# Kernel optimization log

Measured on AMD Instinct MI355X. Metric: run time of the kernel, lower is better.

The kernel has to match this reference:

```python
import jax, jax.numpy as jnp
import numpy as np

B, N, NIN = 32, 128, 64
MSG_HID, MSG_OUT, N_HID, N_OUT = 256, 64, 256, 64
E = N * (N - 1)  # fully connected, no self loops


def setup_inputs() -> dict:
    key = jax.random.key(0)
    ks = jax.random.split(key, 12)

    # one-hot incidence matrices (NRI convention)
    off = np.ones((N, N), dtype=np.float32) - np.eye(N, dtype=np.float32)
    recv_idx, send_idx = np.where(off)
    eye = np.eye(N, dtype=np.float32)
    rel_rec = jnp.asarray(eye[recv_idx])    # [E, N]
    rel_send = jnp.asarray(eye[send_idx])   # [E, N]

    s = 0.05
    inp = {
        "inputs": jax.random.normal(ks[0], (B, N, NIN), jnp.float32),
        "rel_rec": rel_rec,
        "rel_send": rel_send,
        "rel_types": jax.random.uniform(ks[1], (B, E, 2), jnp.float32),
        "msg_fc1_w": jax.random.normal(ks[2], (MSG_HID, 2 * NIN), jnp.float32) * s,
        "msg_fc1_b": jnp.zeros((MSG_HID,), jnp.float32),
        "msg_fc2_w": jax.random.normal(ks[3], (MSG_OUT, MSG_HID), jnp.float32) * s,
        "msg_fc2_b": jnp.zeros((MSG_OUT,), jnp.float32),
        "out_fc1_w": jax.random.normal(ks[4], (N_HID, MSG_OUT), jnp.float32) * s,
        "out_fc1_b": jnp.zeros((N_HID,), jnp.float32),
        "out_fc2_w": jax.random.normal(ks[5], (N_HID, N_HID), jnp.float32) * s,
        "out_fc2_b": jnp.zeros((N_HID,), jnp.float32),
        "out_fc3_w": jax.random.normal(ks[6], (N_OUT, N_HID), jnp.float32) * s,
        "out_fc3_b": jnp.zeros((N_OUT,), jnp.float32),
    }
    return inp


def reference(inputs, rel_rec, rel_send, rel_types,
              msg_fc1_w, msg_fc1_b, msg_fc2_w, msg_fc2_b,
              out_fc1_w, out_fc1_b, out_fc2_w, out_fc2_b,
              out_fc3_w, out_fc3_b):
    # node2edge: gather sender / receiver node features via one-hot matmul
    senders = jnp.einsum('en,bnf->bef', rel_send, inputs)    # [B,E,NIN]
    receivers = jnp.einsum('en,bnf->bef', rel_rec, inputs)   # [B,E,NIN]
    pre_msg = jnp.concatenate([senders, receivers], axis=-1)  # [B,E,2*NIN]

    all_msgs = jnp.zeros(pre_msg.shape[:2] + (MSG_OUT,), pre_msg.dtype)
    for i in range(2):  # edge-type loop (shared weights, as in the original)
        msg = jax.nn.relu(pre_msg @ msg_fc1_w.T + msg_fc1_b)
        msg = jax.nn.relu(msg @ msg_fc2_w.T + msg_fc2_b)
        all_msgs = all_msgs + msg * rel_types[:, :, i:i + 1]

    # edge2node: scatter-add messages to receiving nodes
    agg_msgs = jnp.einsum('bem,en->bnm', all_msgs, rel_rec)   # [B,N,MSG_OUT]

    pred = jax.nn.relu(agg_msgs @ out_fc1_w.T + out_fc1_b)
    pred = jax.nn.relu(pred @ out_fc2_w.T + out_fc2_b)
    pred = pred @ out_fc3_w.T + out_fc3_b                      # [B,N,N_OUT]
    return pred
```

## Files before the change

kernel.cpp:

```cpp
#include <hip/hip_runtime.h>

#define BB 32
#define NN_ 128
#define NIN 64
#define MH 256
#define MO 64
#define NH 256
#define NO 64
#define EDGES 16256

typedef __attribute__((ext_vector_type(8))) short short8;
typedef __attribute__((ext_vector_type(4))) float f32x4;
typedef __attribute__((ext_vector_type(2))) float f32x2;


static __device__ __forceinline__ unsigned short f2bf(float f) {
    unsigned u = __float_as_uint(f);
    u = (u + 0x7fffu + ((u >> 16) & 1u)) >> 16;
    return (unsigned short)u;
}

static __device__ __forceinline__ unsigned bf_pack(float lo, float hi) {
    return __builtin_amdgcn_perm(__float_as_uint(hi) + 0x8000u,
                                 __float_as_uint(lo) + 0x8000u, 0x07060302u);
}

static __device__ __forceinline__ short8 pack8(float4 f0, float4 f1) {
    uint4 u;
    u.x = bf_pack(f0.x, f0.y);
    u.y = bf_pack(f0.z, f0.w);
    u.z = bf_pack(f1.x, f1.y);
    u.w = bf_pack(f1.z, f1.w);
    return __builtin_bit_cast(short8, u);
}

static __device__ __forceinline__ void unpack8v(uint4 u, f32x2* f) {
    f[0] = (f32x2){__uint_as_float(u.x << 16), __uint_as_float(u.x & 0xffff0000u)};
    f[1] = (f32x2){__uint_as_float(u.y << 16), __uint_as_float(u.y & 0xffff0000u)};
    f[2] = (f32x2){__uint_as_float(u.z << 16), __uint_as_float(u.z & 0xffff0000u)};
    f[3] = (f32x2){__uint_as_float(u.w << 16), __uint_as_float(u.w & 0xffff0000u)};
}

static __device__ __forceinline__ short8 buildAv(const f32x2* s, const f32x2* p) {
    uint4 u;
    #pragma unroll
    for (int i = 0; i < 4; ++i) {
        f32x2 h = s[i] + p[i];
        h = __builtin_elementwise_max(h, (f32x2){0.f, 0.f});
        ((unsigned*)&u)[i] = bf_pack(h.x, h.y);
    }
    return __builtin_bit_cast(short8, u);
}

__global__ __launch_bounds__(256) void prep_kernel(
    const float* __restrict__ x, const float* __restrict__ W1,
    const float* __restrict__ b1, const float* __restrict__ W2,
    const float* __restrict__ O1, const float* __restrict__ O2,
    const float* __restrict__ O3,
    unsigned short* __restrict__ psb, unsigned short* __restrict__ prb,
    unsigned short* __restrict__ w2b, unsigned short* __restrict__ o1b,
    unsigned short* __restrict__ o2b, unsigned short* __restrict__ o3b)
{
    int blk = blockIdx.x;
    int t = threadIdx.x;
    if (blk < 256) {
        int row0 = blk << 4;
        int b = blk >> 3;
        int w = t >> 6, lane = t & 63, ml = lane & 15, q = lane >> 4;

        short8 aX[2];
        #pragma unroll
        for (int s = 0; s < 2; ++s) {
            const float* base = x + (size_t)(row0 + ml) * NIN + s * 32 + q * 8;
            aX[s] = pack8(*(const float4*)base, *(const float4*)(base + 4));
        }

        #pragma unroll
        for (int half = 0; half < 2; ++half) {
            #pragma unroll
            for (int nt = 0; nt < 4; ++nt) {
                int col = w * 64 + nt * 16 + ml;
                const float* wrow = W1 + (size_t)col * (2 * NIN) + half * 64 + q * 8;
                f32x4 acc = (f32x4){0.f, 0.f, 0.f, 0.f};
                #pragma unroll
                for (int s = 0; s < 2; ++s) {
                    short8 bw = pack8(*(const float4*)(wrow + 32 * s),
                                      *(const float4*)(wrow + 32 * s + 4));
                    acc = __builtin_amdgcn_mfma_f32_16x16x32_bf16(aX[s], bw, acc, 0, 0, 0);
                }
                if (half == 0) {
                    #pragma unroll
                    for (int reg = 0; reg < 4; ++reg) {
                        int n = (row0 + q * 4 + reg) & 127;
                        psb[((size_t)(b * 32 + (col >> 3)) * NN_ + n) * 8 + (col & 7)]
                            = f2bf(acc[reg]);
                    }
                } else {
                    float bv = b1[col];
                    #pragma unroll
                    for (int reg = 0; reg < 4; ++reg) {
                        int n = (row0 + q * 4 + reg) & 127;
                        prb[((size_t)(b * NN_) + n) * MH + col] = f2bf(acc[reg] + bv);
                    }
                }
            }
        }
    } else if (blk < 320) {
        int i = ((blk - 256) << 8) + t;
        int kc4 = i >> 9, rem = i & 511;
        int n = rem >> 3, k7 = i & 7;
        w2b[i] = f2bf(W2[n * MH + kc4 * 8 + k7]);
    } else {
        int i = ((blk - 320) << 8) + t;
        if (i < 16384)       o1b[i]         = f2bf(O1[i]);
        else if (i < 81920)  o2b[i - 16384] = f2bf(O2[i - 16384]);
        else                 o3b[i - 81920] = f2bf(O3[i - 81920]);
    }
}

__global__ __launch_bounds__(256, 4) void edge_kernel(
    const float* __restrict__ rt, const float* __restrict__ b2,
    const unsigned short* __restrict__ psb, const unsigned short* __restrict__ prb,
    const unsigned short* __restrict__ w2b, float* __restrict__ agg)
{
    int blk = blockIdx.x;
    int b = blk & 31;
    int r0 = (blk >> 5) << 1;
    int tid = threadIdx.x;
    int w = tid >> 6, lane = tid & 63, ml = lane & 15, q = lane >> 4;

    __shared__ float rtw_lds[2][128];
    __shared__ float red[2][4][64];
    {
        int rr = tid >> 7, s = tid & 127;
        int r = r0 + rr;
        float v = 0.f;
        if (s != r) {
            int e = r * 127 + s - (s > r ? 1 : 0);
            const float* p = rt + ((size_t)(b * EDGES + e)) * 2;
            v = __builtin_nontemporal_load(p) + __builtin_nontemporal_load(p + 1);
        }
        rtw_lds[rr][s] = v;
    }
    __syncthreads();

    int slot0 = 32 * w + ml;
    int slot1 = slot0 + 16;

    const uint4* ps4 = (const uint4*)psb + (size_t)b * (32 * NN_);
    const uint4* pr4_0 = (const uint4*)(prb + ((size_t)(b * NN_ + r0)) * MH);
    const uint4* pr4_1 = (const uint4*)(prb + ((size_t)(b * NN_ + r0 + 1)) * MH);
    const uint4* w24 = (const uint4*)w2b;

    f32x4 acc[2][2][4];
    #pragma unroll
    for (int rr = 0; rr < 2; ++rr)
        #pragma unroll
        for (int mt = 0; mt < 2; ++mt)
            #pragma unroll
            for (int nt = 0; nt < 4; ++nt)
                acc[rr][mt][nt] = (f32x4){0.f, 0.f, 0.f, 0.f};

    #pragma unroll
    for (int kc = 0; kc < 8; ++kc) {
        int kc4 = 4 * kc + q;
        uint4 us0 = ps4[kc4 * NN_ + slot0];
        uint4 us1 = ps4[kc4 * NN_ + slot1];
        uint4 up0 = pr4_0[kc4];
        uint4 up1 = pr4_1[kc4];

        f32x2 s0f[4], s1f[4], p0f[4], p1f[4];
        unpack8v(us0, s0f); unpack8v(us1, s1f);
        unpack8v(up0, p0f); unpack8v(up1, p1f);

        short8 a00 = buildAv(s0f, p0f);
        short8 a01 = buildAv(s1f, p0f);
        short8 a10 = buildAv(s0f, p1f);
        short8 a11 = buildAv(s1f, p1f);

        #pragma unroll
        for (int nt = 0; nt < 4; ++nt) {
            short8 bw = __builtin_bit_cast(short8, w24[kc4 * 64 + 16 * nt + ml]);
            acc[0][0][nt] = __builtin_amdgcn_mfma_f32_16x16x32_bf16(a00, bw, acc[0][0][nt], 0, 0, 0);
            acc[0][1][nt] = __builtin_amdgcn_mfma_f32_16x16x32_bf16(a01, bw, acc[0][1][nt], 0, 0, 0);
            acc[1][0][nt] = __builtin_amdgcn_mfma_f32_16x16x32_bf16(a10, bw, acc[1][0][nt], 0, 0, 0);
            acc[1][1][nt] = __builtin_amdgcn_mfma_f32_16x16x32_bf16(a11, bw, acc[1][1][nt], 0, 0, 0);
        }
    }

    float b2c[4];
    #pragma unroll
    for (int nt = 0; nt < 4; ++nt) b2c[nt] = b2[16 * nt + ml];

    #pragma unroll
    for (int rr = 0; rr < 2; ++rr) {
        float colsum[4] = {0.f, 0.f, 0.f, 0.f};
        #pragma unroll
        for (int mt = 0; mt < 2; ++mt) {
            int slotbase = 32 * w + 16 * mt + 4 * q;
            #pragma unroll
            for (int reg = 0; reg < 4; ++reg) {
                float rw = rtw_lds[rr][slotbase + reg];
                #pragma unroll
                for (int nt = 0; nt < 4; ++nt)
                    colsum[nt] += fmaxf(acc[rr][mt][nt][reg] + b2c[nt], 0.f) * rw;
            }
        }
        #pragma unroll
        for (int nt = 0; nt < 4; ++nt) {
            colsum[nt] += __shfl_xor(colsum[nt], 16);
            colsum[nt] += __shfl_xor(colsum[nt], 32);
        }
        if (lane < 16) {
            #pragma unroll
            for (int nt = 0; nt < 4; ++nt) red[rr][w][16 * nt + ml] = colsum[nt];
        }
    }
    __syncthreads();
    if (tid < 128) {
        int rr = tid >> 6, o = tid & 63;
        agg[((size_t)(b * NN_ + r0 + rr)) * MO + o] =
            red[rr][0][o] + red[rr][1][o] + red[rr][2][o] + red[rr][3][o];
    }
}

__global__ __launch_bounds__(256) void node_kernel(
    const float* __restrict__ agg,
    const unsigned short* __restrict__ O1b, const float* __restrict__ b1o,
    const unsigned short* __restrict__ O2b, const float* __restrict__ b2o,
    const unsigned short* __restrict__ O3b, const float* __restrict__ b3o,
    float* __restrict__ out)
{
    int tid = threadIdx.x;
    int w = tid >> 6, lane = tid & 63, ml = lane & 15, q = lane >> 4;
    int row0 = blockIdx.x << 4;

    __shared__ unsigned short h1L[16][264];
    __shared__ unsigned short h2L[16][264];

    short8 aA[2];
    #pragma unroll
    for (int s = 0; s < 2; ++s) {
        const float* base = agg + (size_t)(row0 + ml) * MO + 32 * s + q * 8;
        aA[s] = pack8(*(const float4*)base, *(const float4*)(base + 4));
    }

    #pragma unroll
    for (int nt = 0; nt < 4; ++nt) {
        int ntg = w * 4 + nt;
        f32x4 acc = (f32x4){0.f, 0.f, 0.f, 0.f};
        #pragma unroll
        for (int s = 0; s < 2; ++s) {
            uint4 uw = *(const uint4*)(O1b + (size_t)(ntg * 16 + ml) * 64 + 32 * s + q * 8);
            acc = __builtin_amdgcn_mfma_f32_16x16x32_bf16(
                aA[s], __builtin_bit_cast(short8, uw), acc, 0, 0, 0);
        }
        float bv = b1o[ntg * 16 + ml];
        #pragma unroll
        for (int reg = 0; reg < 4; ++reg)
            h1L[q * 4 + reg][ntg * 16 + ml] = f2bf(fmaxf(acc[reg] + bv, 0.f));
    }
    __syncthreads();

    short8 aH[8];
    #pragma unroll
    for (int ks = 0; ks < 8; ++ks)
        aH[ks] = *(const short8*)&h1L[ml][32 * ks + q * 8];
    #pragma unroll
    for (int nt = 0; nt < 4; ++nt) {
        int ntg = w * 4 + nt;
        const unsigned short* wrow = O2b + (size_t)(ntg * 16 + ml) * NH + q * 8;
        f32x4 acc = (f32x4){0.f, 0.f, 0.f, 0.f};
        #pragma unroll
        for (int ks = 0; ks < 8; ++ks) {
            uint4 uw = *(const uint4*)(wrow + 32 * ks);
            acc = __builtin_amdgcn_mfma_f32_16x16x32_bf16(
                aH[ks], __builtin_bit_cast(short8, uw), acc, 0, 0, 0);
        }
        float bv = b2o[ntg * 16 + ml];
        #pragma unroll
        for (int reg = 0; reg < 4; ++reg)
            h2L[q * 4 + reg][ntg * 16 + ml] = f2bf(fmaxf(acc[reg] + bv, 0.f));
    }
    __syncthreads();

    #pragma unroll
    for (int ks = 0; ks < 8; ++ks)
        aH[ks] = *(const short8*)&h2L[ml][32 * ks + q * 8];
    {
        const unsigned short* wrow = O3b + (size_t)(w * 16 + ml) * NH + q * 8;
        f32x4 acc = (f32x4){0.f, 0.f, 0.f, 0.f};
        #pragma unroll
        for (int ks = 0; ks < 8; ++ks) {
            uint4 uw = *(const uint4*)(wrow + 32 * ks);
            acc = __builtin_amdgcn_mfma_f32_16x16x32_bf16(
                aH[ks], __builtin_bit_cast(short8, uw), acc, 0, 0, 0);
        }
        float bv = b3o[w * 16 + ml];
        #pragma unroll
        for (int reg = 0; reg < 4; ++reg)
            out[(size_t)(row0 + q * 4 + reg) * NO + w * 16 + ml] = acc[reg] + bv;
    }
}

extern "C" void kernel_launch(void* const* d_in, const int* in_sizes, int n_in,
                              void* d_out, int out_size, void* d_ws, size_t ws_size,
                              hipStream_t stream) {
    const float* x   = (const float*)d_in[0];
    const float* rt  = (const float*)d_in[3];
    const float* W1  = (const float*)d_in[4];
    const float* b1  = (const float*)d_in[5];
    const float* W2  = (const float*)d_in[6];
    const float* b2  = (const float*)d_in[7];
    const float* O1  = (const float*)d_in[8];
    const float* b1o = (const float*)d_in[9];
    const float* O2  = (const float*)d_in[10];
    const float* b2o = (const float*)d_in[11];
    const float* O3  = (const float*)d_in[12];
    const float* b3o = (const float*)d_in[13];

    float* ws  = (float*)d_ws;
    unsigned short* psb = (unsigned short*)ws;
    unsigned short* prb = (unsigned short*)(ws + 524288);
    unsigned short* w2b = (unsigned short*)(ws + 1048576);
    float* agg = ws + 1056768;
    unsigned short* o1b = (unsigned short*)(ws + 1318912);
    unsigned short* o2b = (unsigned short*)(ws + 1327104);
    unsigned short* o3b = (unsigned short*)(ws + 1359872);
    float* out = (float*)d_out;

    hipLaunchKernelGGL(prep_kernel, dim3(704), dim3(256), 0, stream,
                       x, W1, b1, W2, O1, O2, O3, psb, prb, w2b, o1b, o2b, o3b);
    hipLaunchKernelGGL(edge_kernel, dim3(2048), dim3(256), 0, stream,
                       rt, b2, psb, prb, w2b, agg);
    hipLaunchKernelGGL(node_kernel, dim3(256), dim3(256), 0, stream,
                       agg, o1b, b1o, o2b, b2o, o3b, b3o, out);
}
```

Baseline: 130.6 us.

## Fuse prep, edge and node kernels into one persistent kernel with grid barriers

New measurement: 308.2 us. 2.36x slower.

```diff
diff --git a/kernel.cpp b/kernel.cpp
--- a/kernel.cpp
+++ b/kernel.cpp
@@ -1,6 +1,5 @@
 #include <hip/hip_runtime.h>
 
-#define BB 32
 #define NN_ 128
 #define NIN 64
 #define MH 256
@@ -8,6 +7,7 @@
 #define NH 256
 #define NO 64
 #define EDGES 16256
+#define GRID 512
 
 typedef __attribute__((ext_vector_type(8))) short short8;
 typedef __attribute__((ext_vector_type(4))) float f32x4;
@@ -52,254 +52,271 @@
     return __builtin_bit_cast(short8, u);
 }
 
-__global__ __launch_bounds__(256) void prep_kernel(
-    const float* __restrict__ x, const float* __restrict__ W1,
-    const float* __restrict__ b1, const float* __restrict__ W2,
-    const float* __restrict__ O1, const float* __restrict__ O2,
-    const float* __restrict__ O3,
+__device__ unsigned g_gen = 0;
+__device__ unsigned g_cnt = 0;
+
+static __device__ __forceinline__ void grid_barrier() {
+    __syncthreads();
+    if (threadIdx.x == 0) {
+        __threadfence();
+        unsigned g = __hip_atomic_load(&g_gen, __ATOMIC_RELAXED, __HIP_MEMORY_SCOPE_AGENT);
+        unsigned my = __hip_atomic_fetch_add(&g_cnt, 1, __ATOMIC_ACQ_REL, __HIP_MEMORY_SCOPE_AGENT);
+        if (my == GRID - 1) {
+            __hip_atomic_store(&g_cnt, 0, __ATOMIC_RELAXED, __HIP_MEMORY_SCOPE_AGENT);
+            __hip_atomic_fetch_add(&g_gen, 1, __ATOMIC_RELEASE, __HIP_MEMORY_SCOPE_AGENT);
+        } else {
+            while (__hip_atomic_load(&g_gen, __ATOMIC_ACQUIRE, __HIP_MEMORY_SCOPE_AGENT) == g)
+                __builtin_amdgcn_s_sleep(8);
+        }
+        __threadfence();
+    }
+    __syncthreads();
+}
+
+__global__ __launch_bounds__(256, 2) void fused_kernel(
+    const float* __restrict__ x, const float* __restrict__ rt,
+    const float* __restrict__ W1, const float* __restrict__ b1,
+    const float* __restrict__ W2, const float* __restrict__ b2,
+    const float* __restrict__ O1, const float* __restrict__ b1o,
+    const float* __restrict__ O2, const float* __restrict__ b2o,
+    const float* __restrict__ O3, const float* __restrict__ b3o,
     unsigned short* __restrict__ psb, unsigned short* __restrict__ prb,
     unsigned short* __restrict__ w2b, unsigned short* __restrict__ o1b,
-    unsigned short* __restrict__ o2b, unsigned short* __restrict__ o3b)
+    unsigned short* __restrict__ o2b, unsigned short* __restrict__ o3b,
+    float* __restrict__ agg, float* __restrict__ out)
 {
     int blk = blockIdx.x;
     int t = threadIdx.x;
+    int w = t >> 6, lane = t & 63, ml = lane & 15, q = lane >> 4;
+
+    __shared__ float rtw_lds[2][128];
+    __shared__ float red[2][4][64];
+    __shared__ unsigned short h1L[16][264];
+    __shared__ unsigned short h2L[16][264];
+
+    for (int vb = blk; vb < 704; vb += GRID) {
+        if (vb < 256) {
+            int row0 = vb << 4;
+            int b = vb >> 3;
+            short8 aX[2];
+            #pragma unroll
+            for (int s = 0; s < 2; ++s) {
+                const float* base = x + (size_t)(row0 + ml) * NIN + s * 32 + q * 8;
+                aX[s] = pack8(*(const float4*)base, *(const float4*)(base + 4));
+            }
+            #pragma unroll
+            for (int half = 0; half < 2; ++half) {
+                #pragma unroll
+                for (int nt = 0; nt < 4; ++nt) {
+                    int col = w * 64 + nt * 16 + ml;
+                    const float* wrow = W1 + (size_t)col * (2 * NIN) + half * 64 + q * 8;
+                    f32x4 acc = (f32x4){0.f, 0.f, 0.f, 0.f};
+                    #pragma unroll
+                    for (int s = 0; s < 2; ++s) {
+                        short8 bw = pack8(*(const float4*)(wrow + 32 * s),
+                                          *(const float4*)(wrow + 32 * s + 4));
+                        acc = __builtin_amdgcn_mfma_f32_16x16x32_bf16(aX[s], bw, acc, 0, 0, 0);
+                    }
+                    if (half == 0) {
+                        #pragma unroll
+                        for (int reg = 0; reg < 4; ++reg) {
+                            int n = (row0 + q * 4 + reg) & 127;
+                            psb[((size_t)(b * 32 + (col >> 3)) * NN_ + n) * 8 + (col & 7)]
+                                = f2bf(acc[reg]);
+                        }
+                    } else {
+                        float bv = b1[col];
+                        #pragma unroll
+                        for (int reg = 0; reg < 4; ++reg) {
+                            int n = (row0 + q * 4 + reg) & 127;
+                            prb[((size_t)(b * NN_) + n) * MH + col] = f2bf(acc[reg] + bv);
+                        }
+                    }
+                }
+            }
+        } else if (vb < 320) {
+            int i = ((vb - 256) << 8) + t;
+            int kc4 = i >> 9, rem = i & 511;
+            int n = rem >> 3, k7 = i & 7;
+            w2b[i] = f2bf(W2[n * MH + kc4 * 8 + k7]);
+        } else {
+            int i = ((vb - 320) << 8) + t;
+            if (i < 16384)       o1b[i]         = f2bf(O1[i]);
+            else if (i < 81920)  o2b[i - 16384] = f2bf(O2[i - 16384]);
+            else                 o3b[i - 81920] = f2bf(O3[i - 81920]);
+        }
+    }
+
+    grid_barrier();
+
+    {
+        int b = blk & 31;
+        const uint4* ps4 = (const uint4*)psb + (size_t)b * (32 * NN_);
+        const uint4* w24 = (const uint4*)w2b;
+        int slot0 = 32 * w + ml;
+        int slot1 = slot0 + 16;
+        float b2c[4];
+        #pragma unroll
+        for (int nt = 0; nt < 4; ++nt) b2c[nt] = b2[16 * nt + ml];
+
+        for (int it = 0; it < 4; ++it) {
+            int vb = blk + GRID * it;
+            int r0 = (vb >> 5) << 1;
+
+            __syncthreads();
+            {
+                int rr = t >> 7, s = t & 127;
+                int r = r0 + rr;
+                float v = 0.f;
+                if (s != r) {
+                    int e = r * 127 + s - (s > r ? 1 : 0);
+                    const float* p = rt + ((size_t)(b * EDGES + e)) * 2;
+                    v = __builtin_nontemporal_load(p) + __builtin_nontemporal_load(p + 1);
+                }
+                rtw_lds[rr][s] = v;
+            }
+            __syncthreads();
+
+            const uint4* pr4_0 = (const uint4*)(prb + ((size_t)(b * NN_ + r0)) * MH);
+            const uint4* pr4_1 = (const uint4*)(prb + ((size_t)(b * NN_ + r0 + 1)) * MH);
+
+            f32x4 acc[2][2][4];
+            #pragma unroll
+            for (int rr = 0; rr < 2; ++rr)
+                #pragma unroll
+                for (int mt = 0; mt < 2; ++mt)
+                    #pragma unroll
+                    for (int nt = 0; nt < 4; ++nt)
+                        acc[rr][mt][nt] = (f32x4){0.f, 0.f, 0.f, 0.f};
+
+            #pragma unroll
+            for (int kc = 0; kc < 8; ++kc) {
+                int kc4 = 4 * kc + q;
+                uint4 us0 = ps4[kc4 * NN_ + slot0];
+                uint4 us1 = ps4[kc4 * NN_ + slot1];
+                uint4 up0 = pr4_0[kc4];
+                uint4 up1 = pr4_1[kc4];
+
+                f32x2 s0f[4], s1f[4], p0f[4], p1f[4];
+                unpack8v(us0, s0f); unpack8v(us1, s1f);
+                unpack8v(up0, p0f); unpack8v(up1, p1f);
+
+                short8 a00 = buildAv(s0f, p0f);
+                short8 a01 = buildAv(s1f, p0f);
+                short8 a10 = buildAv(s0f, p1f);
+                short8 a11 = buildAv(s1f, p1f);
+
+                #pragma unroll
+                for (int nt = 0; nt < 4; ++nt) {
+                    short8 bw = __builtin_bit_cast(short8, w24[kc4 * 64 + 16 * nt + ml]);
+                    acc[0][0][nt] = __builtin_amdgcn_mfma_f32_16x16x32_bf16(a00, bw, acc[0][0][nt], 0, 0, 0);
+                    acc[0][1][nt] = __builtin_amdgcn_mfma_f32_16x16x32_bf16(a01, bw, acc[0][1][nt], 0, 0, 0);
+                    acc[1][0][nt] = __builtin_amdgcn_mfma_f32_16x16x32_bf16(a10, bw, acc[1][0][nt], 0, 0, 0);
+                    acc[1][1][nt] = __builtin_amdgcn_mfma_f32_16x16x32_bf16(a11, bw, acc[1][1][nt], 0, 0, 0);
+                }
+            }
+
+            #pragma unroll
+            for (int rr = 0; rr < 2; ++rr) {
+                float colsum[4] = {0.f, 0.f, 0.f, 0.f};
+                #pragma unroll
+                for (int mt = 0; mt < 2; ++mt) {
+                    int slotbase = 32 * w + 16 * mt + 4 * q;
+                    #pragma unroll
+                    for (int reg = 0; reg < 4; ++reg) {
+                        float rw = rtw_lds[rr][slotbase + reg];
+                        #pragma unroll
+                        for (int nt = 0; nt < 4; ++nt)
+                            colsum[nt] += fmaxf(acc[rr][mt][nt][reg] + b2c[nt], 0.f) * rw;
+                    }
+                }
+                #pragma unroll
+                for (int nt = 0; nt < 4; ++nt) {
+                    colsum[nt] += __shfl_xor(colsum[nt], 16);
+                    colsum[nt] += __shfl_xor(colsum[nt], 32);
+                }
+                if (lane < 16) {
+                    #pragma unroll
+                    for (int nt = 0; nt < 4; ++nt) red[rr][w][16 * nt + ml] = colsum[nt];
+                }
+            }
+            __syncthreads();
+            if (t < 128) {
+                int rr = t >> 6, o = t & 63;
+                agg[((size_t)(b * NN_ + r0 + rr)) * MO + o] =
+                    red[rr][0][o] + red[rr][1][o] + red[rr][2][o] + red[rr][3][o];
+            }
+        }
+    }
+
+    grid_barrier();
+
     if (blk < 256) {
         int row0 = blk << 4;
-        int b = blk >> 3;
-        int w = t >> 6, lane = t & 63, ml = lane & 15, q = lane >> 4;
-
-        short8 aX[2];
+
+        short8 aA[2];
         #pragma unroll
         for (int s = 0; s < 2; ++s) {
-            const float* base = x + (size_t)(row0 + ml) * NIN + s * 32 + q * 8;
-            aX[s] = pack8(*(const float4*)base, *(const float4*)(base + 4));
-        }
-
-        #pragma unroll
-        for (int half = 0; half < 2; ++half) {
-            #pragma unroll
-            for (int nt = 0; nt < 4; ++nt) {
-                int col = w * 64 + nt * 16 + ml;
-                const float* wrow = W1 + (size_t)col * (2 * NIN) + half * 64 + q * 8;
-                f32x4 acc = (f32x4){0.f, 0.f, 0.f, 0.f};
-                #pragma unroll
-                for (int s = 0; s < 2; ++s) {
-                    short8 bw = pack8(*(const float4*)(wrow + 32 * s),
-                                      *(const float4*)(wrow + 32 * s + 4));
-                    acc = __builtin_amdgcn_mfma_f32_16x16x32_bf16(aX[s], bw, acc, 0, 0, 0);
-                }
-                if (half == 0) {
-                    #pragma unroll
-                    for (int reg = 0; reg < 4; ++reg) {
-                        int n = (row0 + q * 4 + reg) & 127;
-                        psb[((size_t)(b * 32 + (col >> 3)) * NN_ + n) * 8 + (col & 7)]
-                            = f2bf(acc[reg]);
-                    }
-                } else {
-                    float bv = b1[col];
-                    #pragma unroll
-                    for (int reg = 0; reg < 4; ++reg) {
-                        int n = (row0 + q * 4 + reg) & 127;
-                        prb[((size_t)(b * NN_) + n) * MH + col] = f2bf(acc[reg] + bv);
-                    }
-                }
-            }
-        }
-    } else if (blk < 320) {
-        int i = ((blk - 256) << 8) + t;
-        int kc4 = i >> 9, rem = i & 511;
-        int n = rem >> 3, k7 = i & 7;
-        w2b[i] = f2bf(W2[n * MH + kc4 * 8 + k7]);
-    } else {
-        int i = ((blk - 320) << 8) + t;
-        if (i < 16384)       o1b[i]         = f2bf(O1[i]);
-        else if (i < 81920)  o2b[i - 16384] = f2bf(O2[i - 16384]);
-        else                 o3b[i - 81920] = f2bf(O3[i - 81920]);
-    }
-}
-
-__global__ __launch_bounds__(256, 4) void edge_kernel(
-    const float* __restrict__ rt, const float* __restrict__ b2,
-    const unsigned short* __restrict__ psb, const unsigned short* __restrict__ prb,
-    const unsigned short* __restrict__ w2b, float* __restrict__ agg)
-{
-    int blk = blockIdx.x;
-    int b = blk & 31;
-    int r0 = (blk >> 5) << 1;
-    int tid = threadIdx.x;
-    int w = tid >> 6, lane = tid & 63, ml = lane & 15, q = lane >> 4;
-
-    __shared__ float rtw_lds[2][128];
-    __shared__ float red[2][4][64];
-    {
-        int rr = tid >> 7, s = tid & 127;
-        int r = r0 + rr;
-        float v = 0.f;
-        if (s != r) {
-            int e = r * 127 + s - (s > r ? 1 : 0);
-            const float* p = rt + ((size_t)(b * EDGES + e)) * 2;
-            v = __builtin_nontemporal_load(p) + __builtin_nontemporal_load(p + 1);
-        }
-        rtw_lds[rr][s] = v;
-    }
-    __syncthreads();
-
-    int slot0 = 32 * w + ml;
-    int slot1 = slot0 + 16;
-
-    const uint4* ps4 = (const uint4*)psb + (size_t)b * (32 * NN_);
-    const uint4* pr4_0 = (const uint4*)(prb + ((size_t)(b * NN_ + r0)) * MH);
-    const uint4* pr4_1 = (const uint4*)(prb + ((size_t)(b * NN_ + r0 + 1)) * MH);
-    const uint4* w24 = (const uint4*)w2b;
-
-    f32x4 acc[2][2][4];
-    #pragma unroll
-    for (int rr = 0; rr < 2; ++rr)
-        #pragma unroll
-        for (int mt = 0; mt < 2; ++mt)
-            #pragma unroll
-            for (int nt = 0; nt < 4; ++nt)
-                acc[rr][mt][nt] = (f32x4){0.f, 0.f, 0.f, 0.f};
-
-    #pragma unroll
-    for (int kc = 0; kc < 8; ++kc) {
-        int kc4 = 4 * kc + q;
-        uint4 us0 = ps4[kc4 * NN_ + slot0];
-        uint4 us1 = ps4[kc4 * NN_ + slot1];
-        uint4 up0 = pr4_0[kc4];
-        uint4 up1 = pr4_1[kc4];
-
-        f32x2 s0f[4], s1f[4], p0f[4], p1f[4];
-        unpack8v(us0, s0f); unpack8v(us1, s1f);
-        unpack8v(up0, p0f); unpack8v(up1, p1f);
-
-        short8 a00 = buildAv(s0f, p0f);
-        short8 a01 = buildAv(s1f, p0f);
-        short8 a10 = buildAv(s0f, p1f);
-        short8 a11 = buildAv(s1f, p1f);
+            const float* base = agg + (size_t)(row0 + ml) * MO + 32 * s + q * 8;
+            aA[s] = pack8(*(const float4*)base, *(const float4*)(base + 4));
+        }
 
         #pragma unroll
         for (int nt = 0; nt < 4; ++nt) {
-            short8 bw = __builtin_bit_cast(short8, w24[kc4 * 64 + 16 * nt + ml]);
-            acc[0][0][nt] = __builtin_amdgcn_mfma_f32_16x16x32_bf16(a00, bw, acc[0][0][nt], 0, 0, 0);
-            acc[0][1][nt] = __builtin_amdgcn_mfma_f32_16x16x32_bf16(a01, bw, acc[0][1][nt], 0, 0, 0);
-            acc[1][0][nt] = __builtin_amdgcn_mfma_f32_16x16x32_bf16(a10, bw, acc[1][0][nt], 0, 0, 0);
-            acc[1][1][nt] = __builtin_amdgcn_mfma_f32_16x16x32_bf16(a11, bw, acc[1][1][nt], 0, 0, 0);
-        }
-    }
-
-    float b2c[4];
-    #pragma unroll
-    for (int nt = 0; nt < 4; ++nt) b2c[nt] = b2[16 * nt + ml];
-
-    #pragma unroll
-    for (int rr = 0; rr < 2; ++rr) {
-        float colsum[4] = {0.f, 0.f, 0.f, 0.f};
-        #pragma unroll
-        for (int mt = 0; mt < 2; ++mt) {
-            int slotbase = 32 * w + 16 * mt + 4 * q;
-            #pragma unroll
-            for (int reg = 0; reg < 4; ++reg) {
-                float rw = rtw_lds[rr][slotbase + reg];
-                #pragma unroll
-                for (int nt = 0; nt < 4; ++nt)
-                    colsum[nt] += fmaxf(acc[rr][mt][nt][reg] + b2c[nt], 0.f) * rw;
-            }
-        }
+            int ntg = w * 4 + nt;
+            f32x4 acc = (f32x4){0.f, 0.f, 0.f, 0.f};
+            #pragma unroll
+            for (int s = 0; s < 2; ++s) {
+                uint4 uw = *(const uint4*)(o1b + (size_t)(ntg * 16 + ml) * 64 + 32 * s + q * 8);
+                acc = __builtin_amdgcn_mfma_f32_16x16x32_bf16(
+                    aA[s], __builtin_bit_cast(short8, uw), acc, 0, 0, 0);
+            }
+            float bv = b1o[ntg * 16 + ml];
+            #pragma unroll
+            for (int reg = 0; reg < 4; ++reg)
+                h1L[q * 4 + reg][ntg * 16 + ml] = f2bf(fmaxf(acc[reg] + bv, 0.f));
+        }
+        __syncthreads();
+
+        short8 aH[8];
+        #pragma unroll
+        for (int ks = 0; ks < 8; ++ks)
+            aH[ks] = *(const short8*)&h1L[ml][32 * ks + q * 8];
         #pragma unroll
         for (int nt = 0; nt < 4; ++nt) {
-            colsum[nt] += __shfl_xor(colsum[nt], 16);
-            colsum[nt] += __shfl_xor(colsum[nt], 32);
-        }
-        if (lane < 16) {
-            #pragma unroll
-            for (int nt = 0; nt < 4; ++nt) red[rr][w][16 * nt + ml] = colsum[nt];
-        }
-    }
-    __syncthreads();
-    if (tid < 128) {
-        int rr = tid >> 6, o = tid & 63;
-        agg[((size_t)(b * NN_ + r0 + rr)) * MO + o] =
-            red[rr][0][o] + red[rr][1][o] + red[rr][2][o] + red[rr][3][o];
-    }
-}
-
-__global__ __launch_bounds__(256) void node_kernel(
-    const float* __restrict__ agg,
-    const unsigned short* __restrict__ O1b, const float* __restrict__ b1o,
-    const unsigned short* __restrict__ O2b, const float* __restrict__ b2o,
-    const unsigned short* __restrict__ O3b, const float* __restrict__ b3o,
-    float* __restrict__ out)
-{
-    int tid = threadIdx.x;
-    int w = tid >> 6, lane = tid & 63, ml = lane & 15, q = lane >> 4;
-    int row0 = blockIdx.x << 4;
-
-    __shared__ unsigned short h1L[16][264];
-    __shared__ unsigned short h2L[16][264];
-
-    short8 aA[2];
-    #pragma unroll
-    for (int s = 0; s < 2; ++s) {
-        const float* base = agg + (size_t)(row0 + ml) * MO + 32 * s + q * 8;
-        aA[s] = pack8(*(const float4*)base, *(const float4*)(base + 4));
-    }
-
-    #pragma unroll
-    for (int nt = 0; nt < 4; ++nt) {
-        int ntg = w * 4 + nt;
-        f32x4 acc = (f32x4){0.f, 0.f, 0.f, 0.f};
-        #pragma unroll
-        for (int s = 0; s < 2; ++s) {
-            uint4 uw = *(const uint4*)(O1b + (size_t)(ntg * 16 + ml) * 64 + 32 * s + q * 8);
-            acc = __builtin_amdgcn_mfma_f32_16x16x32_bf16(
-                aA[s], __builtin_bit_cast(short8, uw), acc, 0, 0, 0);
-        }
-        float bv = b1o[ntg * 16 + ml];
-        #pragma unroll
-        for (int reg = 0; reg < 4; ++reg)
-            h1L[q * 4 + reg][ntg * 16 + ml] = f2bf(fmaxf(acc[reg] + bv, 0.f));
-    }
-    __syncthreads();
-
-    short8 aH[8];
-    #pragma unroll
-    for (int ks = 0; ks < 8; ++ks)
-        aH[ks] = *(const short8*)&h1L[ml][32 * ks + q * 8];
-    #pragma unroll
-    for (int nt = 0; nt < 4; ++nt) {
-        int ntg = w * 4 + nt;
-        const unsigned short* wrow = O2b + (size_t)(ntg * 16 + ml) * NH + q * 8;
-        f32x4 acc = (f32x4){0.f, 0.f, 0.f, 0.f};
-        #pragma unroll
-        for (int ks = 0; ks < 8; ++ks) {
-            uint4 uw = *(const uint4*)(wrow + 32 * ks);
-            acc = __builtin_amdgcn_mfma_f32_16x16x32_bf16(
-                aH[ks], __builtin_bit_cast(short8, uw), acc, 0, 0, 0);
-        }
-        float bv = b2o[ntg * 16 + ml];
-        #pragma unroll
-        for (int reg = 0; reg < 4; ++reg)
-            h2L[q * 4 + reg][ntg * 16 + ml] = f2bf(fmaxf(acc[reg] + bv, 0.f));
-    }
-    __syncthreads();
-
-    #pragma unroll
-    for (int ks = 0; ks < 8; ++ks)
-        aH[ks] = *(const short8*)&h2L[ml][32 * ks + q * 8];
-    {
-        const unsigned short* wrow = O3b + (size_t)(w * 16 + ml) * NH + q * 8;
-        f32x4 acc = (f32x4){0.f, 0.f, 0.f, 0.f};
-        #pragma unroll
-        for (int ks = 0; ks < 8; ++ks) {
-            uint4 uw = *(const uint4*)(wrow + 32 * ks);
-            acc = __builtin_amdgcn_mfma_f32_16x16x32_bf16(
-                aH[ks], __builtin_bit_cast(short8, uw), acc, 0, 0, 0);
-        }
-        float bv = b3o[w * 16 + ml];
-        #pragma unroll
-        for (int reg = 0; reg < 4; ++reg)
-            out[(size_t)(row0 + q * 4 + reg) * NO + w * 16 + ml] = acc[reg] + bv;
+            int ntg = w * 4 + nt;
+            const unsigned short* wrow = o2b + (size_t)(ntg * 16 + ml) * NH + q * 8;
+            f32x4 acc = (f32x4){0.f, 0.f, 0.f, 0.f};
+            #pragma unroll
+            for (int ks = 0; ks < 8; ++ks) {
+                uint4 uw = *(const uint4*)(wrow + 32 * ks);
+                acc = __builtin_amdgcn_mfma_f32_16x16x32_bf16(
+                    aH[ks], __builtin_bit_cast(short8, uw), acc, 0, 0, 0);
+            }
+            float bv = b2o[ntg * 16 + ml];
+            #pragma unroll
+            for (int reg = 0; reg < 4; ++reg)
+                h2L[q * 4 + reg][ntg * 16 + ml] = f2bf(fmaxf(acc[reg] + bv, 0.f));
+        }
+        __syncthreads();
+
+        #pragma unroll
+        for (int ks = 0; ks < 8; ++ks)
+            aH[ks] = *(const short8*)&h2L[ml][32 * ks + q * 8];
+        {
+            const unsigned short* wrow = o3b + (size_t)(w * 16 + ml) * NH + q * 8;
+            f32x4 acc = (f32x4){0.f, 0.f, 0.f, 0.f};
+            #pragma unroll
+            for (int ks = 0; ks < 8; ++ks) {
+                uint4 uw = *(const uint4*)(wrow + 32 * ks);
+                acc = __builtin_amdgcn_mfma_f32_16x16x32_bf16(
+                    aH[ks], __builtin_bit_cast(short8, uw), acc, 0, 0, 0);
+            }
+            float bv = b3o[w * 16 + ml];
+            #pragma unroll
+            for (int reg = 0; reg < 4; ++reg)
+                out[(size_t)(row0 + q * 4 + reg) * NO + w * 16 + ml] = acc[reg] + bv;
+        }
     }
 }
 
@@ -329,10 +346,7 @@
     unsigned short* o3b = (unsigned short*)(ws + 1359872);
     float* out = (float*)d_out;
 
-    hipLaunchKernelGGL(prep_kernel, dim3(704), dim3(256), 0, stream,
-                       x, W1, b1, W2, O1, O2, O3, psb, prb, w2b, o1b, o2b, o3b);
-    hipLaunchKernelGGL(edge_kernel, dim3(2048), dim3(256), 0, stream,
-                       rt, b2, psb, prb, w2b, agg);
-    hipLaunchKernelGGL(node_kernel, dim3(256), dim3(256), 0, stream,
-                       agg, o1b, b1o, o2b, b2o, o3b, b3o, out);
-}
+    hipLaunchKernelGGL(fused_kernel, dim3(GRID), dim3(256), 0, stream,
+                       x, rt, W1, b1, W2, b2, O1, b1o, O2, b2o, O3, b3o,
+                       psb, prb, w2b, o1b, o2b, o3b, agg, out);
+}
```
